# Optimization experiments

Hardware: AMD Instinct MI355X
Metric: run time of the kernel (lower is better)

The kernel has to match this reference:

```python
import jax, jax.numpy as jnp
import numpy as np

B, P, PLOIDY = 8, 5000, 2
NALLELES, NPOS, D = 16, 20000, 64


def setup_inputs() -> dict:
    key = jax.random.key(0)
    k1, k2, k3, k4, k5 = jax.random.split(key, 5)
    alleles = jax.random.randint(k1, (B, P, PLOIDY), 0, NALLELES, dtype=jnp.int32)
    positions = jax.random.randint(k2, (B, P), 0, NPOS, dtype=jnp.int32)
    allele_table = jax.random.normal(k3, (NALLELES, D), dtype=jnp.float32)
    kernel_table = jax.random.normal(k4, (NPOS, D * D), dtype=jnp.float32)
    bias_table = jax.random.normal(k5, (NPOS, D), dtype=jnp.float32)
    return {"alleles": alleles, "positions": positions,
            "allele_table": allele_table, "kernel_table": kernel_table,
            "bias_table": bias_table}


def reference(alleles, positions, allele_table, kernel_table, bias_table):
    # gather allele embeddings and sum over ploidy: [B,P,ploidy,D] -> [B,P,D]
    a = allele_table[alleles].sum(axis=-2)
    # per-position weight matrix: [B,P,D,D]
    kernel = kernel_table[positions].reshape(positions.shape[0], positions.shape[1], D, D)
    bias = bias_table[positions]                       # [B,P,D]
    # batched 1xD @ DxD matmul, fused with bias add
    out = jnp.einsum('bpd,bpde->bpe', a, kernel) + bias
    return out  # activation is None (linear)
```

## Files before the change

kernel.cpp:

```cpp
#include <hip/hip_runtime.h>

#define BB 8
#define PP 5000
#define DD 64
#define NBP (BB * PP)
#define WAVES_PER_BLOCK 4

__global__ __launch_bounds__(256) void allele_embed_kernel(
    const int* __restrict__ alleles,
    const int* __restrict__ positions,
    const float* __restrict__ allele_table,
    const float4* __restrict__ ktab4,
    const float4* __restrict__ btab4,
    float4* __restrict__ out4)
{
    const int wave = threadIdx.x >> 6;
    const int lane = threadIdx.x & 63;
    const int bp   = blockIdx.x * WAVES_PER_BLOCK + wave;

    const int al0 = alleles[bp * 2 + 0];
    const int al1 = alleles[bp * 2 + 1];
    const int pos = positions[bp];

    const float a_full = allele_table[al0 * DD + lane] + allele_table[al1 * DD + lane];

    const float4* __restrict__ krow = ktab4 + (size_t)pos * (DD * DD / 4);
    const int dg = lane >> 4;

    float4 acc = make_float4(0.f, 0.f, 0.f, 0.f);
#pragma unroll
    for (int i = 0; i < 16; ++i) {
        const int d   = i * 4 + dg;
        const float ad = __shfl(a_full, d, 64);
        const float4 kv = krow[i * 64 + lane];
        acc.x += ad * kv.x;
        acc.y += ad * kv.y;
        acc.z += ad * kv.z;
        acc.w += ad * kv.w;
    }

#pragma unroll
    for (int off = 16; off <= 32; off <<= 1) {
        acc.x += __shfl_xor(acc.x, off, 64);
        acc.y += __shfl_xor(acc.y, off, 64);
        acc.z += __shfl_xor(acc.z, off, 64);
        acc.w += __shfl_xor(acc.w, off, 64);
    }

    if (lane < 16) {
        const float4 bv = btab4[(size_t)pos * (DD / 4) + lane];
        acc.x += bv.x;
        acc.y += bv.y;
        acc.z += bv.z;
        acc.w += bv.w;
        out4[(size_t)bp * (DD / 4) + lane] = acc;
    }
}

extern "C" void kernel_launch(void* const* d_in, const int* in_sizes, int n_in,
                              void* d_out, int out_size, void* d_ws, size_t ws_size,
                              hipStream_t stream) {
    const int*   alleles      = (const int*)d_in[0];
    const int*   positions    = (const int*)d_in[1];
    const float* allele_table = (const float*)d_in[2];
    const float4* ktab4       = (const float4*)d_in[3];
    const float4* btab4       = (const float4*)d_in[4];
    float4* out4              = (float4*)d_out;

    const int grid = NBP / WAVES_PER_BLOCK;
    allele_embed_kernel<<<grid, WAVES_PER_BLOCK * 64, 0, stream>>>(
        alleles, positions, allele_table, ktab4, btab4, out4);
}
```

Before: 456.7 us.

## Bucket-sort work items by position for kernel-row cache reuse

Adds a histogram, scan and scatter pass that groups batch-position items by position bucket (16 positions per bucket). The main kernel then processes items in that order, with blocks interleaved across XCDs, so repeated positions that read the same 16 KB kernel-table row run close together in time and can hit in L2 or MALL. Each item still does the same work. The cost is three extra kernel launches plus a memset, atomic contention in the histogram, and an extra indirection load per wave.

```diff
diff --git a/kernel.cpp b/kernel.cpp
--- a/kernel.cpp
+++ b/kernel.cpp
@@ -4,7 +4,57 @@
 #define PP 5000
 #define DD 64
 #define NBP (BB * PP)
+#define NPOSC 20000
 #define WAVES_PER_BLOCK 4
+#define GRID_MAIN (NBP / WAVES_PER_BLOCK)
+
+#define BSHIFT 4
+#define NBUCKET 1250
+#define NBUCKET_PAD 1280
+
+__global__ __launch_bounds__(256) void hist_kernel(
+    const int* __restrict__ positions, int* __restrict__ hist)
+{
+    const int tid = blockIdx.x * 256 + threadIdx.x;
+    if (tid < NBP) atomicAdd(&hist[positions[tid] >> BSHIFT], 1);
+}
+
+__global__ __launch_bounds__(256) void scan_kernel(
+    const int* __restrict__ hist, int* __restrict__ offs)
+{
+    __shared__ int lsum[256];
+    const int t = threadIdx.x;
+    const int base = t * 5;
+    int v[5];
+#pragma unroll
+    for (int j = 0; j < 5; ++j)
+        v[j] = (base + j < NBUCKET) ? hist[base + j] : 0;
+    int run = 0;
+#pragma unroll
+    for (int j = 0; j < 5; ++j) { int x = v[j]; v[j] = run; run += x; }
+    lsum[t] = run;
+    __syncthreads();
+    if (t == 0) {
+        int acc = 0;
+        for (int i = 0; i < 256; ++i) { int x = lsum[i]; lsum[i] = acc; acc += x; }
+    }
+    __syncthreads();
+#pragma unroll
+    for (int j = 0; j < 5; ++j)
+        if (base + j < NBUCKET) offs[base + j] = lsum[t] + v[j];
+}
+
+__global__ __launch_bounds__(256) void scatter_kernel(
+    const int* __restrict__ positions, int* __restrict__ offs,
+    int* __restrict__ order)
+{
+    const int tid = blockIdx.x * 256 + threadIdx.x;
+    if (tid < NBP) {
+        const int b = positions[tid] >> BSHIFT;
+        const int idx = atomicAdd(&offs[b], 1);
+        order[idx] = tid;
+    }
+}
 
 __global__ __launch_bounds__(256) void allele_embed_kernel(
     const int* __restrict__ alleles,
@@ -12,11 +62,13 @@
     const float* __restrict__ allele_table,
     const float4* __restrict__ ktab4,
     const float4* __restrict__ btab4,
+    const int* __restrict__ order,
     float4* __restrict__ out4)
 {
     const int wave = threadIdx.x >> 6;
     const int lane = threadIdx.x & 63;
-    const int bp   = blockIdx.x * WAVES_PER_BLOCK + wave;
+    const int work = (blockIdx.x & 7) * (GRID_MAIN / 8) + (blockIdx.x >> 3);
+    const int bp   = order[work * WAVES_PER_BLOCK + wave];
 
     const int al0 = alleles[bp * 2 + 0];
     const int al1 = alleles[bp * 2 + 1];
@@ -30,7 +82,7 @@
     float4 acc = make_float4(0.f, 0.f, 0.f, 0.f);
 #pragma unroll
     for (int i = 0; i < 16; ++i) {
-        const int d   = i * 4 + dg;
+        const int d    = i * 4 + dg;
         const float ad = __shfl(a_full, d, 64);
         const float4 kv = krow[i * 64 + lane];
         acc.x += ad * kv.x;
@@ -67,7 +119,17 @@
     const float4* btab4       = (const float4*)d_in[4];
     float4* out4              = (float4*)d_out;
 
-    const int grid = NBP / WAVES_PER_BLOCK;
-    allele_embed_kernel<<<grid, WAVES_PER_BLOCK * 64, 0, stream>>>(
-        alleles, positions, allele_table, ktab4, btab4, out4);
+    int* hist  = (int*)d_ws;
+    int* offs  = hist + NBUCKET_PAD;
+    int* order = offs + NBUCKET_PAD;
+
+    hipMemsetAsync(hist, 0, NBUCKET_PAD * sizeof(int), stream);
+
+    const int gprep = (NBP + 255) / 256;
+    hist_kernel<<<gprep, 256, 0, stream>>>(positions, hist);
+    scan_kernel<<<1, 256, 0, stream>>>(hist, offs);
+    scatter_kernel<<<gprep, 256, 0, stream>>>(positions, offs, order);
+
+    allele_embed_kernel<<<GRID_MAIN, WAVES_PER_BLOCK * 64, 0, stream>>>(
+        alleles, positions, allele_table, ktab4, btab4, order, out4);
 }
```

After: 452.4 us. About the same (-0.9%).
